# Kernel tuning notes

Measured on AMD Instinct MI355X. Metric: run time of the kernel, lower is better.

## Reference

```python
import jax, jax.numpy as jnp
import numpy as np

HEADS = 8
TQ, QH, QW = 4, 16, 16
TK, KH, KW = 4, 16, 16
DIM = 64


def setup_inputs() -> dict:
    key = jax.random.key(0)
    k1, k2, k3, k4, k5 = jax.random.split(key, 5)
    return {
        "query": jax.random.normal(k1, (4, HEADS, TQ * QH * QW, DIM), dtype=jnp.float32),
        "scores": jax.random.normal(k2, (4, HEADS, TQ * QH * QW, TK * KH * KW), dtype=jnp.float32),
        "height_embeddings": jax.random.normal(k3, (2 * (max(QH, KH) - 1) + 1, DIM), dtype=jnp.float32),
        "width_embeddings": jax.random.normal(k4, (2 * (max(QW, KW) - 1) + 1, DIM), dtype=jnp.float32),
        "time_embeddings": jax.random.normal(k5, (2 * (max(TQ, TK) - 1) + 1, DIM), dtype=jnp.float32),
    }


def _rel_dist(q_n, k_n):
    # matches torch: ratios are both 1 when q_n == k_n
    q_ratio = round(max(k_n / q_n, 1.0))
    k_ratio = round(max(q_n / k_n, 1.0))
    d = jnp.arange(q_n)[:, None] * q_ratio - jnp.arange(k_n)[None, :] * k_ratio
    return d + (k_n - 1) * k_ratio  # [q_n, k_n] int indices


def reference(query, scores, height_embeddings, width_embeddings, time_embeddings):
    Rh = height_embeddings[_rel_dist(QH, KH)]  # [QH, KH, DIM]
    Rw = width_embeddings[_rel_dist(QW, KW)]   # [QW, KW, DIM]
    Rt = time_embeddings[_rel_dist(TQ, TK)]    # [TQ, TK, DIM]

    q = query.reshape(-1, HEADS, TQ, QH, QW, DIM)
    rel_h = jnp.einsum('bNthwc,hkc->bNthwk', q, Rh)  # [B,N,T,H,W,KH]
    rel_w = jnp.einsum('bNthwc,wkc->bNthwk', q, Rw)  # [B,N,T,H,W,KW]
    rel_t = jnp.einsum('bNthwc,tkc->bNthwk', q, Rt)  # [B,N,T,H,W,TK]

    s = scores.reshape(-1, HEADS, TQ, QH, QW, TK, KH, KW)
    s = (s
         + rel_h[:, :, :, :, :, None, :, None]
         + rel_w[:, :, :, :, :, None, None, :]
         + rel_t[:, :, :, :, :, :, None, None])
    return s.reshape(-1, HEADS, TQ * QH * QW, TK * KH * KW)
```

## Files before the change

### kernel.cpp

```cpp
#include <hip/hip_runtime.h>

#define NHEADS 8
#define TQ 4
#define QH 16
#define QW 16
#define TK 4
#define KH 16
#define KW 16
#define DIM 64
#define BATCH 4

__global__ __launch_bounds__(256) void relpos_kernel(
    const float* __restrict__ query,
    const float* __restrict__ scores,
    const float* __restrict__ hemb,
    const float* __restrict__ wemb,
    const float* __restrict__ temb,
    float* __restrict__ out)
{
    const int row = blockIdx.x;
    const int pos = row & 1023;
    const int t = pos >> 8;
    const int h = (pos >> 4) & 15;
    const int w = pos & 15;

    __shared__ float q[DIM];
    __shared__ float rel[36];

    const int tid = threadIdx.x;
    if (tid < DIM) q[tid] = query[(size_t)row * DIM + tid];
    __syncthreads();

    if (tid < 36) {
        const float* emb;
        int r;
        if (tid < 16)      { emb = hemb; r = h - tid + 15; }
        else if (tid < 32) { emb = wemb; r = w - (tid - 16) + 15; }
        else               { emb = temb; r = t - (tid - 32) + 3; }
        const float4* e4 = (const float4*)(emb + (size_t)r * DIM);
        float acc = 0.f;
#pragma unroll
        for (int c = 0; c < DIM / 4; ++c) {
            float4 ev = e4[c];
            acc += q[4 * c + 0] * ev.x + q[4 * c + 1] * ev.y
                 + q[4 * c + 2] * ev.z + q[4 * c + 3] * ev.w;
        }
        rel[tid] = acc;
    }
    __syncthreads();

    const int base = tid << 2;
    const int tk  = base >> 8;
    const int kh  = (base >> 4) & 15;
    const int kw0 = base & 15;

    const float add_hk = rel[kh] + rel[32 + tk];
    const float4 s = *(const float4*)(scores + (size_t)row * 1024 + base);
    float4 o;
    o.x = s.x + add_hk + rel[16 + kw0 + 0];
    o.y = s.y + add_hk + rel[16 + kw0 + 1];
    o.z = s.z + add_hk + rel[16 + kw0 + 2];
    o.w = s.w + add_hk + rel[16 + kw0 + 3];
    *(float4*)(out + (size_t)row * 1024 + base) = o;
}

extern "C" void kernel_launch(void* const* d_in, const int* in_sizes, int n_in,
                              void* d_out, int out_size, void* d_ws, size_t ws_size,
                              hipStream_t stream) {
    const float* query  = (const float*)d_in[0];
    const float* scores = (const float*)d_in[1];
    const float* hemb   = (const float*)d_in[2];
    const float* wemb   = (const float*)d_in[3];
    const float* temb   = (const float*)d_in[4];
    float* out = (float*)d_out;

    const int rows = BATCH * NHEADS * TQ * QH * QW;
    relpos_kernel<<<dim3(rows), dim3(256), 0, stream>>>(query, scores, hemb, wemb, temb, out);
}
```

Measured before the change: 259.0 us.

## Process four rows per block and prefetch scores before the embedding dot products

Each block now handles four consecutive query rows, and 144 threads compute the relative-position dot products for all four. The scores loads are issued at kernel entry, before the dot products and barrier, so global memory latency overlaps with the embedding computation. The shared-memory query staging and one barrier are dropped, with threads reading the query directly from global memory. There are four times fewer blocks and more registers per thread to hold the prefetched float4s.

```diff
diff --git a/kernel.cpp b/kernel.cpp
--- a/kernel.cpp
+++ b/kernel.cpp
@@ -18,34 +18,39 @@
     const float* __restrict__ temb,
     float* __restrict__ out)
 {
-    const int row = blockIdx.x;
-    const int pos = row & 1023;
-    const int t = pos >> 8;
-    const int h = (pos >> 4) & 15;
-    const int w = pos & 15;
+    const int tid  = threadIdx.x;
+    const int row0 = blockIdx.x << 2;
+    const int pos  = row0 & 1023;
+    const int t  = pos >> 8;
+    const int h  = (pos >> 4) & 15;
+    const int w0 = pos & 15;
 
-    __shared__ float q[DIM];
-    __shared__ float rel[36];
+    const float4* sc4 = (const float4*)(scores + (size_t)row0 * 1024);
+    float4 s0 = sc4[tid];
+    float4 s1 = sc4[256 + tid];
+    float4 s2 = sc4[512 + tid];
+    float4 s3 = sc4[768 + tid];
 
-    const int tid = threadIdx.x;
-    if (tid < DIM) q[tid] = query[(size_t)row * DIM + tid];
-    __syncthreads();
+    __shared__ float rel[4][36];
 
-    if (tid < 36) {
+    if (tid < 144) {
+        const int r = tid / 36;
+        const int j = tid - r * 36;
         const float* emb;
-        int r;
-        if (tid < 16)      { emb = hemb; r = h - tid + 15; }
-        else if (tid < 32) { emb = wemb; r = w - (tid - 16) + 15; }
-        else               { emb = temb; r = t - (tid - 32) + 3; }
-        const float4* e4 = (const float4*)(emb + (size_t)r * DIM);
+        int e;
+        if (j < 16)      { emb = hemb; e = h - j + 15; }
+        else if (j < 32) { emb = wemb; e = (w0 + r) - (j - 16) + 15; }
+        else             { emb = temb; e = t - (j - 32) + 3; }
+        const float4* e4 = (const float4*)(emb + (size_t)e * DIM);
+        const float4* q4 = (const float4*)(query + (size_t)(row0 + r) * DIM);
         float acc = 0.f;
 #pragma unroll
         for (int c = 0; c < DIM / 4; ++c) {
+            float4 qv = q4[c];
             float4 ev = e4[c];
-            acc += q[4 * c + 0] * ev.x + q[4 * c + 1] * ev.y
-                 + q[4 * c + 2] * ev.z + q[4 * c + 3] * ev.w;
+            acc += qv.x * ev.x + qv.y * ev.y + qv.z * ev.z + qv.w * ev.w;
         }
-        rel[tid] = acc;
+        rel[r][j] = acc;
     }
     __syncthreads();
 
@@ -54,14 +59,18 @@
     const int kh  = (base >> 4) & 15;
     const int kw0 = base & 15;
 
-    const float add_hk = rel[kh] + rel[32 + tk];
-    const float4 s = *(const float4*)(scores + (size_t)row * 1024 + base);
-    float4 o;
-    o.x = s.x + add_hk + rel[16 + kw0 + 0];
-    o.y = s.y + add_hk + rel[16 + kw0 + 1];
-    o.z = s.z + add_hk + rel[16 + kw0 + 2];
-    o.w = s.w + add_hk + rel[16 + kw0 + 3];
-    *(float4*)(out + (size_t)row * 1024 + base) = o;
+    float4* o4 = (float4*)(out + (size_t)row0 * 1024);
+#pragma unroll
+    for (int r = 0; r < 4; ++r) {
+        const float4 s = (r == 0) ? s0 : (r == 1) ? s1 : (r == 2) ? s2 : s3;
+        const float a = rel[r][kh] + rel[r][32 + tk];
+        float4 o;
+        o.x = s.x + a + rel[r][16 + kw0 + 0];
+        o.y = s.y + a + rel[r][16 + kw0 + 1];
+        o.z = s.z + a + rel[r][16 + kw0 + 2];
+        o.w = s.w + a + rel[r][16 + kw0 + 3];
+        o4[r * 256 + tid] = o;
+    }
 }
 
 extern "C" void kernel_launch(void* const* d_in, const int* in_sizes, int n_in,
@@ -75,5 +84,5 @@
     float* out = (float*)d_out;
 
     const int rows = BATCH * NHEADS * TQ * QH * QW;
-    relpos_kernel<<<dim3(rows), dim3(256), 0, stream>>>(query, scores, hemb, wemb, temb, out);
+    relpos_kernel<<<dim3(rows / 4), dim3(256), 0, stream>>>(query, scores, hemb, wemb, temb, out);
 }
```

Result: faster. 251.0 us (-3.1%).

## Assign one wavefront per row with early nontemporal score loads

Applied to the files above, without the earlier changes.

Each 256-thread block now handles four rows, one 64-lane wavefront per row, so each lane processes four float4 chunks. The scores loads are issued before the small dot products, which hides their latency behind the embedding reduction. Block-wide __syncthreads is replaced by a wave barrier, and query is read directly from global memory instead of staged in shared memory. Nontemporal loads and stores target the streaming traffic, at the cost of more registers per thread.

```diff
diff --git a/kernel.cpp b/kernel.cpp
--- a/kernel.cpp
+++ b/kernel.cpp
@@ -9,8 +9,11 @@
 #define KW 16
 #define DIM 64
 #define BATCH 4
+#define ROWS (BATCH * NHEADS * TQ * QH * QW)
 
-__global__ __launch_bounds__(256) void relpos_kernel(
+typedef float f4 __attribute__((ext_vector_type(4)));
+
+__global__ __launch_bounds__(256) void relpos_fused(
     const float* __restrict__ query,
     const float* __restrict__ scores,
     const float* __restrict__ hemb,
@@ -18,50 +21,72 @@
     const float* __restrict__ temb,
     float* __restrict__ out)
 {
-    const int row = blockIdx.x;
-    const int pos = row & 1023;
+    const int lane = threadIdx.x & 63;
+    const int wid  = threadIdx.x >> 6;
+    const int row  = (blockIdx.x << 2) + wid;
+    const int pos  = row & 1023;
     const int t = pos >> 8;
     const int h = (pos >> 4) & 15;
     const int w = pos & 15;
 
-    __shared__ float q[DIM];
-    __shared__ float rel[36];
+    const f4* sc4 = (const f4*)(scores + (size_t)row * 1024);
+    f4 s0 = __builtin_nontemporal_load(&sc4[lane]);
+    f4 s1 = __builtin_nontemporal_load(&sc4[64 + lane]);
+    f4 s2 = __builtin_nontemporal_load(&sc4[128 + lane]);
+    f4 s3 = __builtin_nontemporal_load(&sc4[192 + lane]);
 
-    const int tid = threadIdx.x;
-    if (tid < DIM) q[tid] = query[(size_t)row * DIM + tid];
-    __syncthreads();
+    __shared__ float rel[4][40];
+    if (lane < 36) {
+        const float* emb;
+        int e;
+        if (lane < 16)      { emb = hemb; e = h - lane + 15; }
+        else if (lane < 32) { emb = wemb; e = w - (lane - 16) + 15; }
+        else                { emb = temb; e = t - (lane - 32) + 3; }
+        const f4* e4 = (const f4*)(emb + (size_t)e * DIM);
+        const f4* q4 = (const f4*)(query + (size_t)row * DIM);
+        float a0 = 0.f, a1 = 0.f, a2 = 0.f, a3 = 0.f;
+#pragma unroll
+        for (int c = 0; c < DIM / 4; c += 4) {
+            f4 qa = q4[c + 0], ea = e4[c + 0];
+            f4 qb = q4[c + 1], eb = e4[c + 1];
+            f4 qc = q4[c + 2], ec = e4[c + 2];
+            f4 qd = q4[c + 3], ed = e4[c + 3];
+            a0 += qa.x * ea.x + qa.y * ea.y + qa.z * ea.z + qa.w * ea.w;
+            a1 += qb.x * eb.x + qb.y * eb.y + qb.z * eb.z + qb.w * eb.w;
+            a2 += qc.x * ec.x + qc.y * ec.y + qc.z * ec.z + qc.w * ec.w;
+            a3 += qd.x * ed.x + qd.y * ed.y + qd.z * ed.z + qd.w * ed.w;
+        }
+        rel[wid][lane] = (a0 + a1) + (a2 + a3);
+    }
+    __builtin_amdgcn_wave_barrier();
 
-    if (tid < 36) {
-        const float* emb;
-        int r;
-        if (tid < 16)      { emb = hemb; r = h - tid + 15; }
-        else if (tid < 32) { emb = wemb; r = w - (tid - 16) + 15; }
-        else               { emb = temb; r = t - (tid - 32) + 3; }
-        const float4* e4 = (const float4*)(emb + (size_t)r * DIM);
-        float acc = 0.f;
-#pragma unroll
-        for (int c = 0; c < DIM / 4; ++c) {
-            float4 ev = e4[c];
-            acc += q[4 * c + 0] * ev.x + q[4 * c + 1] * ev.y
-                 + q[4 * c + 2] * ev.z + q[4 * c + 3] * ev.w;
-        }
-        rel[tid] = acc;
+    const int kh  = lane >> 2;
+    const int kw0 = (lane & 3) << 2;
+    const float bh = rel[wid][kh];
+    const f4 bw = *(const f4*)&rel[wid][16 + kw0];
+    const f4 bt = *(const f4*)&rel[wid][32];
+
+    f4* o4 = (f4*)(out + (size_t)row * 1024);
+    {
+        const float a = bh + bt.x;
+        f4 o = s0 + a;  o += bw;
+        __builtin_nontemporal_store(o, &o4[lane]);
     }
-    __syncthreads();
-
-    const int base = tid << 2;
-    const int tk  = base >> 8;
-    const int kh  = (base >> 4) & 15;
-    const int kw0 = base & 15;
-
-    const float add_hk = rel[kh] + rel[32 + tk];
-    const float4 s = *(const float4*)(scores + (size_t)row * 1024 + base);
-    float4 o;
-    o.x = s.x + add_hk + rel[16 + kw0 + 0];
-    o.y = s.y + add_hk + rel[16 + kw0 + 1];
-    o.z = s.z + add_hk + rel[16 + kw0 + 2];
-    o.w = s.w + add_hk + rel[16 + kw0 + 3];
-    *(float4*)(out + (size_t)row * 1024 + base) = o;
+    {
+        const float a = bh + bt.y;
+        f4 o = s1 + a;  o += bw;
+        __builtin_nontemporal_store(o, &o4[64 + lane]);
+    }
+    {
+        const float a = bh + bt.z;
+        f4 o = s2 + a;  o += bw;
+        __builtin_nontemporal_store(o, &o4[128 + lane]);
+    }
+    {
+        const float a = bh + bt.w;
+        f4 o = s3 + a;  o += bw;
+        __builtin_nontemporal_store(o, &o4[192 + lane]);
+    }
 }
 
 extern "C" void kernel_launch(void* const* d_in, const int* in_sizes, int n_in,
@@ -74,6 +99,6 @@
     const float* temb   = (const float*)d_in[4];
     float* out = (float*)d_out;
 
-    const int rows = BATCH * NHEADS * TQ * QH * QW;
-    relpos_kernel<<<dim3(rows), dim3(256), 0, stream>>>(query, scores, hemb, wemb, temb, out);
+    relpos_fused<<<dim3(ROWS / 4), dim3(256), 0, stream>>>(
+        query, scores, hemb, wemb, temb, out);
 }
```

Measured after the change: 258.0 us. No clear change (-0.4%).
